# Kernel optimization log

Hardware: AMD Instinct MI355X
Metric: run time of the kernel (lower is better)

## Reference

```python
import jax, jax.numpy as jnp
import numpy as np

N = 16384

def setup_inputs() -> dict:
    key = jax.random.key(0)
    k1, k2 = jax.random.split(key)
    y_true = jax.random.uniform(k1, (N,), dtype=jnp.float32)
    y_pred = jax.random.normal(k2, (N,), dtype=jnp.float32)
    return {"y_true": y_true, "y_pred": y_pred}

def reference(y_true, y_pred):
    t = y_true.reshape(-1)  # [N]
    p = y_pred.reshape(-1)  # [N]
    # sigmoid of pairwise product p_i * p_j  -> [N, N]
    preds_matrix = jax.nn.sigmoid(p[:, None] * p[None, :])
    # relu(t_i - t_j)  -> [N, N]
    max_value = jnp.maximum(t[:, None] - t[None, :], 0.0)
    cost = -jnp.mean(preds_matrix * max_value)
    return cost
```

## Files before the change

### kernel.cpp

```cpp
#include <hip/hip_runtime.h>
#include <math.h>


#define TB 64
#define PB 192
#define NBC 32
#define NBL 6
#define NIC 8
#define NBLK (NBC * NIC)
#define NTHR 256
#define PLO (-5.0f)
#define PHI (5.0f)

__global__ __launch_bounds__(NTHR, 2) void auc_partials(
    const float* __restrict__ t, const float* __restrict__ p,
    float* __restrict__ slots, int N)
{
    __shared__ float sW[TB][NBL + 2];
    __shared__ float sP[TB][NBL + 2];
    __shared__ float sM[NBL][TB + 1];
    __shared__ float s_red[4];

    const int bid = blockIdx.x;
    const int bc  = bid >> 3;
    const int ic  = bid & 7;
    const int B0  = bc * NBL;
    const int tid = threadIdx.x;

    for (int idx = tid; idx < TB * (NBL + 2); idx += NTHR) {
        (&sW[0][0])[idx] = 0.0f;
        (&sP[0][0])[idx] = 0.0f;
    }
    __syncthreads();

    const float pscale = (float)(PB - 1) / (PHI - PLO);
    const int itersA = N / (NTHR * 4);
    for (int it = 0; it < itersA; ++it) {
        const int j4 = (it * NTHR + tid) * 4;
        const float4 tv = *(const float4*)(t + j4);
        const float4 pv = *(const float4*)(p + j4);
        const float te[4] = {tv.x, tv.y, tv.z, tv.w};
        const float pe[4] = {pv.x, pv.y, pv.z, pv.w};
#pragma unroll
        for (int e = 0; e < 4; ++e) {
            float x = (pe[e] - PLO) * pscale;
            x = fminf(fmaxf(x, 0.0f), (float)(PB - 1) - 1e-4f);
            const int b0 = (int)x;
            const float f = x - (float)b0;
            const int tau = min(max((int)(te[e] * (float)TB), 0), TB - 1);
            const int c = b0 - B0 + 1;
            if ((unsigned)c <= (unsigned)NBL) {
                const float w0 = 1.0f - f;
                atomicAdd(&sW[tau][c],     w0);
                atomicAdd(&sP[tau][c],     w0 * te[e]);
                atomicAdd(&sW[tau][c + 1], f);
                atomicAdd(&sP[tau][c + 1], f * te[e]);
            }
        }
    }
    __syncthreads();

    {
        const int wv = tid >> 6, lane = tid & 63;
        for (int cc = wv; cc < NBL; cc += 4) {
            const float w = sW[lane][cc + 1];
            const float q = sP[lane][cc + 1];
            float wi = w, qi = q;
#pragma unroll
            for (int off = 1; off < 64; off <<= 1) {
                const float wn = __shfl_up(wi, off, 64);
                const float qn = __shfl_up(qi, off, 64);
                if (lane >= off) { wi += wn; qi += qn; }
            }
            const float Wtot = __shfl(wi, 63, 64);
            const float Ptot = __shfl(qi, 63, 64);
            const float A = wi - w;
            const float B = qi - q;
            const float g = (float)lane * (1.0f / (float)TB);
            sM[cc][lane] = g * (2.0f * A - Wtot) + (Ptot - 2.0f * B);
            if (lane == 63) sM[cc][TB] = Wtot - Ptot;
        }
    }
    __syncthreads();

    const float h = (PHI - PLO) / (float)(PB - 1);
    const float q0 = PLO + (float)B0 * h;
    const int i0 = ic * (N / NIC);
    float acc = 0.0f;
    const int itersC = (N / NIC) / (NTHR * 4);
    for (int it = 0; it < itersC; ++it) {
        const int i4 = i0 + (it * NTHR + tid) * 4;
        const float4 tv = *(const float4*)(t + i4);
        const float4 pv = *(const float4*)(p + i4);
        const float te[4] = {tv.x, tv.y, tv.z, tv.w};
        const float pe[4] = {pv.x, pv.y, pv.z, pv.w};
#pragma unroll
        for (int e = 0; e < 4; ++e) {
            const float c = pe[e] * -1.44269504088896340736f;
            float x = te[e] * (float)TB;
            const int k = min((int)x, TB - 1);
            const float f = x - (float)k;
#pragma unroll
            for (int cc = 0; cc < NBL; ++cc) {
                const float m0 = sM[cc][k];
                const float m1 = sM[cc][k + 1];
                const float m  = fmaf(f, m1 - m0, m0);
                const float qb = q0 + (float)cc * h;
                const float ex = __builtin_amdgcn_exp2f(c * qb);
                const float sg = __builtin_amdgcn_rcpf(1.0f + ex);
                acc = fmaf(sg, m, acc);
            }
        }
    }

#pragma unroll
    for (int off = 32; off > 0; off >>= 1)
        acc += __shfl_down(acc, off, 64);
    if ((tid & 63) == 0) s_red[tid >> 6] = acc;
    __syncthreads();
    if (tid == 0)
        slots[bid] = s_red[0] + s_red[1] + s_red[2] + s_red[3];
}

__global__ __launch_bounds__(NTHR) void auc_reduce(
    const float* __restrict__ slots, float* __restrict__ out, float scale)
{
    __shared__ float s_red[4];
    const int tid = threadIdx.x;
    float v = slots[tid];
#pragma unroll
    for (int off = 32; off > 0; off >>= 1)
        v += __shfl_down(v, off, 64);
    if ((tid & 63) == 0) s_red[tid >> 6] = v;
    __syncthreads();
    if (tid == 0)
        out[0] = (s_red[0] + s_red[1] + s_red[2] + s_red[3]) * scale;
}

extern "C" void kernel_launch(void* const* d_in, const int* in_sizes, int n_in,
                              void* d_out, int out_size, void* d_ws, size_t ws_size,
                              hipStream_t stream) {
    const float* y_true = (const float*)d_in[0];
    const float* y_pred = (const float*)d_in[1];
    float* out = (float*)d_out;
    float* slots = (float*)d_ws;
    int N = in_sizes[0];
    float scale = -0.5f / ((float)N * (float)N);

    auc_partials<<<NBLK, NTHR, 0, stream>>>(y_true, y_pred, slots, N);
    auc_reduce<<<1, NTHR, 0, stream>>>(slots, out, scale);
}
```

Baseline: 70.33 us.

## Build histogram once in separate slice kernel instead of per-block rebinning

Previously each of the 256 blocks scanned all N inputs to build its own local (tau, bin) histogram slice in shared memory. Now a new kernel splits the input into 16 slices, and each slice block bins its part into a full global histogram using global atomics. The main kernel then sums the 16 slice histograms for only its 6 bins. This removes the redundant full-input scan from every block, at the cost of an extra launch, global atomics and a global-memory round trip through the workspace.

```diff
diff --git a/kernel.cpp b/kernel.cpp
--- a/kernel.cpp
+++ b/kernel.cpp
@@ -4,6 +4,8 @@
 
 #define TB 64
 #define PB 192
+#define NS 16
+#define SLICE (2 * TB * PB)
 #define NBC 32
 #define NBL 6
 #define NIC 8
@@ -12,31 +14,23 @@
 #define PLO (-5.0f)
 #define PHI (5.0f)
 
-__global__ __launch_bounds__(NTHR, 2) void auc_partials(
+__global__ __launch_bounds__(NTHR) void bin_slices(
     const float* __restrict__ t, const float* __restrict__ p,
-    float* __restrict__ slots, int N)
+    float* __restrict__ hist, int N)
 {
-    __shared__ float sW[TB][NBL + 2];
-    __shared__ float sP[TB][NBL + 2];
-    __shared__ float sM[NBL][TB + 1];
-    __shared__ float s_red[4];
+    const int s   = blockIdx.x;
+    const int tid = threadIdx.x;
+    float* base = hist + s * SLICE;
 
-    const int bid = blockIdx.x;
-    const int bc  = bid >> 3;
-    const int ic  = bid & 7;
-    const int B0  = bc * NBL;
-    const int tid = threadIdx.x;
-
-    for (int idx = tid; idx < TB * (NBL + 2); idx += NTHR) {
-        (&sW[0][0])[idx] = 0.0f;
-        (&sP[0][0])[idx] = 0.0f;
-    }
+    const float4 z = {0.0f, 0.0f, 0.0f, 0.0f};
+    for (int i = tid; i < SLICE / 4; i += NTHR)
+        ((float4*)base)[i] = z;
     __syncthreads();
 
     const float pscale = (float)(PB - 1) / (PHI - PLO);
-    const int itersA = N / (NTHR * 4);
+    const int itersA = N / (NS * NTHR * 4);
     for (int it = 0; it < itersA; ++it) {
-        const int j4 = (it * NTHR + tid) * 4;
+        const int j4 = s * (N / NS) + (it * NTHR + tid) * 4;
         const float4 tv = *(const float4*)(t + j4);
         const float4 pv = *(const float4*)(p + j4);
         const float te[4] = {tv.x, tv.y, tv.z, tv.w};
@@ -48,23 +42,51 @@
             const int b0 = (int)x;
             const float f = x - (float)b0;
             const int tau = min(max((int)(te[e] * (float)TB), 0), TB - 1);
-            const int c = b0 - B0 + 1;
-            if ((unsigned)c <= (unsigned)NBL) {
-                const float w0 = 1.0f - f;
-                atomicAdd(&sW[tau][c],     w0);
-                atomicAdd(&sP[tau][c],     w0 * te[e]);
-                atomicAdd(&sW[tau][c + 1], f);
-                atomicAdd(&sP[tau][c + 1], f * te[e]);
-            }
+            float* w = base + tau * PB + b0;
+            atomicAdd(w,     1.0f - f);
+            atomicAdd(w + 1, f);
+            float* q = w + TB * PB;
+            atomicAdd(q,     (1.0f - f) * te[e]);
+            atomicAdd(q + 1, f * te[e]);
         }
+    }
+}
+
+__global__ __launch_bounds__(NTHR, 2) void auc_main(
+    const float* __restrict__ t, const float* __restrict__ p,
+    const float* __restrict__ hist, float* __restrict__ slots, int N)
+{
+    __shared__ float sW[TB][NBL + 1];
+    __shared__ float sP[TB][NBL + 1];
+    __shared__ float sM[NBL][TB + 1];
+    __shared__ float s_red[4];
+
+    const int bid = blockIdx.x;
+    const int bc  = bid >> 3;
+    const int ic  = bid & 7;
+    const int B0  = bc * NBL;
+    const int tid = threadIdx.x;
+
+    for (int tgt = tid; tgt < 2 * TB * NBL; tgt += NTHR) {
+        int r = tgt, isP = 0;
+        if (r >= TB * NBL) { isP = 1; r -= TB * NBL; }
+        const int tau = r / NBL;
+        const int cc  = r - tau * NBL;
+        const float* g = hist + isP * (TB * PB) + tau * PB + B0 + cc;
+        float a = 0.0f;
+#pragma unroll
+        for (int s2 = 0; s2 < NS; ++s2)
+            a += g[s2 * SLICE];
+        if (isP) sP[tau][cc] = a;
+        else     sW[tau][cc] = a;
     }
     __syncthreads();
 
     {
         const int wv = tid >> 6, lane = tid & 63;
         for (int cc = wv; cc < NBL; cc += 4) {
-            const float w = sW[lane][cc + 1];
-            const float q = sP[lane][cc + 1];
+            const float w = sW[lane][cc];
+            const float q = sP[lane][cc];
             float wi = w, qi = q;
 #pragma unroll
             for (int off = 1; off < 64; off <<= 1) {
@@ -143,10 +165,12 @@
     const float* y_true = (const float*)d_in[0];
     const float* y_pred = (const float*)d_in[1];
     float* out = (float*)d_out;
-    float* slots = (float*)d_ws;
+    float* hist = (float*)d_ws;
+    float* slots = hist + NS * SLICE;
     int N = in_sizes[0];
     float scale = -0.5f / ((float)N * (float)N);
 
-    auc_partials<<<NBLK, NTHR, 0, stream>>>(y_true, y_pred, slots, N);
+    bin_slices<<<NS, NTHR, 0, stream>>>(y_true, y_pred, hist, N);
+    auc_main<<<NBLK, NTHR, 0, stream>>>(y_true, y_pred, hist, slots, N);
     auc_reduce<<<1, NTHR, 0, stream>>>(slots, out, scale);
 }
```

After: 73.46 us. 1.04x slower.
